# Optimization experiments

Measured on AMD Instinct MI355X. Metric: run time of the kernel, lower is better.

## Reference

```python
import jax, jax.numpy as jnp
import numpy as np

N_NODES = 50000
N_EDGES = 1_600_000
D_IN, D_HID, D_OUT, K = 128, 50, 10, 5


def setup_inputs() -> dict:
    key = jax.random.key(0)
    ks = jax.random.split(key, 6)
    x = jax.random.normal(ks[0], (N_NODES, D_IN), dtype=jnp.float32)
    edge_index = jax.random.randint(ks[1], (2, N_EDGES), 0, N_NODES, dtype=jnp.int64)
    cheb_w = jax.random.normal(ks[2], (K, D_IN, D_HID), dtype=jnp.float32) * 0.05
    cheb_b = jax.random.normal(ks[3], (D_HID,), dtype=jnp.float32) * 0.05
    fc_w = jax.random.normal(ks[4], (D_HID, D_OUT), dtype=jnp.float32) * 0.1
    fc_b = jax.random.normal(ks[5], (D_OUT,), dtype=jnp.float32) * 0.1
    return {"x": x, "edge_index": edge_index, "cheb_w": cheb_w,
            "cheb_b": cheb_b, "fc_w": fc_w, "fc_b": fc_b}


def reference(x, edge_index, cheb_w, cheb_b, fc_w, fc_b):
    # ChebConv (PyG, normalization='sym', lambda_max=2.0):
    # L_hat = 2L/lambda_max - I = -D^{-1/2} A D^{-1/2} (zero diagonal)
    row, col = edge_index[0], edge_index[1]
    n = x.shape[0]
    deg = jax.ops.segment_sum(jnp.ones_like(row, dtype=x.dtype), row, num_segments=n)
    dinv = jnp.where(deg > 0, jax.lax.rsqrt(jnp.maximum(deg, 1.0)), 0.0)
    w = -dinv[row] * dinv[col]  # [E] edge weights of L_hat

    def prop(h):  # L_hat @ h via gather-scale-scatter
        return jax.ops.segment_sum(w[:, None] * h[col], row, num_segments=n)

    tx0 = x
    tx1 = prop(x)
    out = jnp.einsum('ni,io->no', tx0, cheb_w[0]) + jnp.einsum('ni,io->no', tx1, cheb_w[1])
    for k in range(2, K):
        tx2 = 2.0 * prop(tx1) - tx0
        out = out + jnp.einsum('ni,io->no', tx2, cheb_w[k])
        tx0, tx1 = tx1, tx2
    out = out + cheb_b

    h = jax.nn.relu(out)
    logits = h @ fc_w + fc_b
    return jax.nn.log_softmax(logits, axis=1)
```

## Files before the change

kernel.cpp:

```cpp
#include <hip/hip_runtime.h>
#include <hip/hip_fp16.h>

#define N_NODES 50000
#define N_EDGES 1600000
#define D_IN    128
#define D_HID   50
#define D_OUT   10
#define K_CHEB  5

#define P1_BLOCKS 256
#define EPB       (N_EDGES / P1_BLOCKS)
#define NBUCK2    256
#define NB_USED2  196
#define BCAP2     96

#define WH_ELEMS  (K_CHEB * 64 * D_IN)
#define WH_BLOCKS ((WH_ELEMS + 255) / 256)
#define XH_BLOCKS (N_NODES * D_IN / 8 / 256)

#define VROW      64
#define VSTRIDE   ((size_t)(N_NODES + 1) * VROW)

#define NGROUP    (N_NODES / 16)
#define VG_SPAN   512
#define VG_WAVES  (K_CHEB * VG_SPAN)
#define VG_BLOCKS (VG_WAVES / 4)

typedef _Float16 half8_t __attribute__((ext_vector_type(8)));
typedef float    f32x4_t __attribute__((ext_vector_type(4)));


__global__ __launch_bounds__(256) void prep_kernel(const float* __restrict__ x,
                                                   const float* __restrict__ W,
                                                   __half* __restrict__ xh,
                                                   __half* __restrict__ Wh,
                                                   __half* __restrict__ u,
                                                   __half* __restrict__ b1,
                                                   __half* __restrict__ b3,
                                                   __half* __restrict__ b2,
                                                   float* __restrict__ dinv) {
    int tid = threadIdx.x;
    int blk = blockIdx.x;
    if (blk < XH_BLOCKS) {
        size_t base = ((size_t)blk * 256 + tid) * 8;
        float4 a = *(const float4*)(x + base);
        float4 b = *(const float4*)(x + base + 4);
        half8_t h;
        h[0] = (_Float16)a.x; h[1] = (_Float16)a.y;
        h[2] = (_Float16)a.z; h[3] = (_Float16)a.w;
        h[4] = (_Float16)b.x; h[5] = (_Float16)b.y;
        h[6] = (_Float16)b.z; h[7] = (_Float16)b.w;
        *(half8_t*)(xh + base) = h;
    } else if (blk < XH_BLOCKS + WH_BLOCKS) {
        int idx = (blk - XH_BLOCKS) * 256 + tid;
        if (idx < WH_ELEMS) {
            int i = idx & 127;
            int n = (idx >> 7) & 63;
            int t = idx >> 13;
            float vv = (n < D_HID) ? W[t * D_IN * D_HID + i * D_HID + n] : 0.f;
            Wh[idx] = __float2half(vv);
        }
    } else {
        if (tid < VROW) {
            __half z = __float2half(0.f);
            u[4 * VSTRIDE + (size_t)N_NODES * VROW + tid] = z;
            b1[(size_t)N_NODES * VROW + tid] = z;
            b3[(size_t)N_NODES * VROW + tid] = z;
            b2[(size_t)N_NODES * VROW + tid] = z;
        }
        if (tid == 64) dinv[N_NODES] = 0.f;
    }
}

__global__ __launch_bounds__(256) void fused_kernel(const int* __restrict__ row,
                                                    const int* __restrict__ col,
                                                    unsigned int* __restrict__ store,
                                                    int* __restrict__ bcnt,
                                                    const __half* __restrict__ xh,
                                                    const __half* __restrict__ Wh,
                                                    __half* __restrict__ u) {
    __shared__ int cnt[NBUCK2];
    int tid = threadIdx.x;
    int blk = blockIdx.x;
    if (blk < VG_BLOCKS) {
        int lane = tid & 63;
        int wv = __builtin_amdgcn_readfirstlane(tid >> 6);
        int w = blk * 4 + wv;
        int t = w / VG_SPAN;
        int idx = w - t * VG_SPAN;
        int m = lane & 15;
        int quad = lane >> 4;

        const __half* Wt = Wh + t * (64 * D_IN);
        half8_t afr[4][4];
        #pragma unroll
        for (int ks = 0; ks < 4; ++ks) {
            int ko = ks * 32 + quad * 8;
            #pragma unroll
            for (int jt = 0; jt < 4; ++jt)
                afr[ks][jt] = *(const half8_t*)(Wt + (jt * 16 + m) * D_IN + ko);
        }

        __half* ut = u + t * VSTRIDE;

        half8_t pf[4];
        int g = idx;
        {
            const __half* xr = xh + (size_t)(g * 16 + m) * D_IN;
            #pragma unroll
            for (int ks = 0; ks < 4; ++ks)
                pf[ks] = *(const half8_t*)(xr + ks * 32 + quad * 8);
        }

        for (; g < NGROUP; g += VG_SPAN) {
            int node = g * 16 + m;
            half8_t bfr[4];
            #pragma unroll
            for (int ks = 0; ks < 4; ++ks) bfr[ks] = pf[ks];
            int gn = g + VG_SPAN;
            if (gn < NGROUP) {
                const __half* xr = xh + (size_t)(gn * 16 + m) * D_IN;
                #pragma unroll
                for (int ks = 0; ks < 4; ++ks)
                    pf[ks] = *(const half8_t*)(xr + ks * 32 + quad * 8);
            }
            f32x4_t acc[4];
            #pragma unroll
            for (int jt = 0; jt < 4; ++jt) acc[jt] = (f32x4_t)0.f;
            #pragma unroll
            for (int ks = 0; ks < 4; ++ks)
                #pragma unroll
                for (int jt = 0; jt < 4; ++jt)
                    acc[jt] = __builtin_amdgcn_mfma_f32_16x16x32_f16(afr[ks][jt], bfr[ks], acc[jt], 0, 0, 0);
            __half* dst = ut + (size_t)node * VROW + quad * 4;
            #pragma unroll
            for (int jt = 0; jt < 4; ++jt) {
                __half2 h0 = __float22half2_rn(make_float2(acc[jt][0], acc[jt][1]));
                __half2 h1 = __float22half2_rn(make_float2(acc[jt][2], acc[jt][3]));
                uint2 uu;
                uu.x = *(unsigned int*)&h0;
                uu.y = *(unsigned int*)&h1;
                *(uint2*)(dst + jt * 16) = uu;
            }
        }
        return;
    }
    int blk2 = blk - VG_BLOCKS;
    cnt[tid] = 0;
    __syncthreads();
    int base = blk2 * EPB;
    size_t sb = (size_t)blk2 * (NBUCK2 * BCAP2);
    for (int i = tid; i < EPB; i += 256) {
        int r = row[base + i];
        int c = col[base + i];
        int b = r >> 8;
        int pos = atomicAdd(&cnt[b], 1);
        if (pos >= BCAP2) pos = BCAP2 - 1;
        store[sb + b * BCAP2 + pos] = ((unsigned int)(r & 255) << 16) | (unsigned int)c;
    }
    __syncthreads();
    bcnt[blk2 * NBUCK2 + tid] = cnt[tid];
}

__global__ __launch_bounds__(512) void pass2_kernel(const unsigned int* __restrict__ store,
                                                    const int* __restrict__ bcnt,
                                                    int* __restrict__ row_start,
                                                    float* __restrict__ dinv,
                                                    float* __restrict__ dinv2,
                                                    float* __restrict__ sdeg,
                                                    int* __restrict__ ewc) {
    __shared__ int hist[256];
    __shared__ int off[256];
    __shared__ int fill[256];
    __shared__ int sb_part[512];
    __shared__ int pscan[256];
    __shared__ int s_bbase;
    int tid = threadIdx.x;
    int b = blockIdx.x;

    {
        int bt = tid & 255, seg = tid >> 8;
        int sum = 0;
        for (int s = seg * 128; s < seg * 128 + 128; ++s) sum += bcnt[s * NBUCK2 + bt];
        sb_part[tid] = sum;
    }
    __syncthreads();
    if (tid < 256) pscan[tid] = sb_part[tid] + sb_part[256 + tid];
    __syncthreads();
    for (int o = 1; o < 256; o <<= 1) {
        int vv = (tid < 256 && tid >= o) ? pscan[tid - o] : 0;
        __syncthreads();
        if (tid < 256) pscan[tid] += vv;
        __syncthreads();
    }
    if (tid == 0) {
        s_bbase = (b == 0) ? 0 : pscan[b - 1];
        if (b == 0) row_start[N_NODES] = pscan[255];
    }
    if (tid < 256) hist[tid] = 0;
    __syncthreads();
    int bbase_b = s_bbase;

    int strip = tid >> 1;
    int sub   = tid & 1;
    int sn = bcnt[strip * NBUCK2 + b];
    size_t sb = (size_t)strip * (NBUCK2 * BCAP2) + b * BCAP2;
    for (int i = sub; i < sn; i += 2)
        atomicAdd(&hist[store[sb + i] >> 16], 1);
    __syncthreads();
    int d = (tid < 256) ? hist[tid] : 0;
    if (tid < 256) off[tid] = d;
    __syncthreads();
    for (int o = 1; o < 256; o <<= 1) {
        int vv = (tid < 256 && tid >= o) ? off[tid - o] : 0;
        __syncthreads();
        if (tid < 256) off[tid] += vv;
        __syncthreads();
    }
    if (tid < 256) {
        int excl = off[tid] - d + bbase_b;
        hist[tid] = excl;
        fill[tid] = 0;
        int r = (b << 8) + tid;
        if (r < N_NODES) {
            row_start[r] = excl;
            float fd = (float)d;
            dinv[r]  = d ? rsqrtf(fd)  : 0.f;
            dinv2[r] = d ? (1.f / fd)  : 0.f;
            sdeg[r]  = d ? sqrtf(fd)   : 0.f;
        }
    }
    __syncthreads();
    for (int i = sub; i < sn; i += 2) {
        unsigned int vv = store[sb + i];
        int rl = vv >> 16;
        int c = vv & 0xffff;
        int p = atomicAdd(&fill[rl], 1);
        ewc[hist[rl] + p] = c;
    }
}

template<int SCALE_SRC, int DO_SUB, int SCALE_SUB>
__global__ __launch_bounds__(512) void prop_kernel(const int* __restrict__ row_start,
                                                   const int* __restrict__ ewc,
                                                   const float* __restrict__ dinv2,
                                                   const float* __restrict__ dinv,
                                                   const __half* __restrict__ src,
                                                   const __half* __restrict__ addv,
                                                   const __half* __restrict__ subv,
                                                   float alphaM,
                                                   __half* __restrict__ dst) {
    int tid = threadIdx.x;
    int lane = tid & 63;
    int wv = __builtin_amdgcn_readfirstlane(tid >> 6);
    int r = blockIdx.x * 8 + wv;
    int e0 = row_start[r], e1 = row_start[r + 1];
    float fac = -alphaM * dinv2[r];
    int l = lane & 7;
    int g = lane >> 3;
    const uint4* src16 = (const uint4*)src;
    float ac[8];
    #pragma unroll
    for (int j = 0; j < 8; ++j) ac[j] = 0.f;
    for (int e = e0; e < e1; e += 32) {
        #pragma unroll
        for (int i = 0; i < 4; ++i) {
            int base = e + 8 * i;
            int cl = ewc[base + g];
            if (base + g >= e1) cl = N_NODES;
            uint4 uu = src16[(size_t)cl * 8 + l];
            float2 f0 = __half22float2(*(__half2*)&uu.x);
            float2 f1 = __half22float2(*(__half2*)&uu.y);
            float2 f2 = __half22float2(*(__half2*)&uu.z);
            float2 f3 = __half22float2(*(__half2*)&uu.w);
            if (SCALE_SRC) {
                float dc = dinv[cl];
                ac[0] = fmaf(dc, f0.x, ac[0]); ac[1] = fmaf(dc, f0.y, ac[1]);
                ac[2] = fmaf(dc, f1.x, ac[2]); ac[3] = fmaf(dc, f1.y, ac[3]);
                ac[4] = fmaf(dc, f2.x, ac[4]); ac[5] = fmaf(dc, f2.y, ac[5]);
                ac[6] = fmaf(dc, f3.x, ac[6]); ac[7] = fmaf(dc, f3.y, ac[7]);
            } else {
                ac[0] += f0.x; ac[1] += f0.y; ac[2] += f1.x; ac[3] += f1.y;
                ac[4] += f2.x; ac[5] += f2.y; ac[6] += f3.x; ac[7] += f3.y;
            }
        }
    }
    #pragma unroll
    for (int k = 8; k <= 32; k <<= 1) {
        #pragma unroll
        for (int j = 0; j < 8; ++j) ac[j] += __shfl_xor(ac[j], k);
    }
    if (g == 0) {
        float sa = dinv[r];
        size_t o = (size_t)r * 8 + l;
        uint4 av = ((const uint4*)addv)[o];
        float2 av0 = __half22float2(*(__half2*)&av.x);
        float2 av1 = __half22float2(*(__half2*)&av.y);
        float2 av2 = __half22float2(*(__half2*)&av.z);
        float2 av3 = __half22float2(*(__half2*)&av.w);
        float r0 = fmaf(sa, av0.x, fac * ac[0]);
        float r1 = fmaf(sa, av0.y, fac * ac[1]);
        float r2 = fmaf(sa, av1.x, fac * ac[2]);
        float r3 = fmaf(sa, av1.y, fac * ac[3]);
        float r4 = fmaf(sa, av2.x, fac * ac[4]);
        float r5 = fmaf(sa, av2.y, fac * ac[5]);
        float r6 = fmaf(sa, av3.x, fac * ac[6]);
        float r7 = fmaf(sa, av3.y, fac * ac[7]);
        if (DO_SUB) {
            float ss = SCALE_SUB ? dinv[r] : 1.f;
            uint4 sv = ((const uint4*)subv)[o];
            float2 sv0 = __half22float2(*(__half2*)&sv.x);
            float2 sv1 = __half22float2(*(__half2*)&sv.y);
            float2 sv2 = __half22float2(*(__half2*)&sv.z);
            float2 sv3 = __half22float2(*(__half2*)&sv.w);
            r0 = fmaf(-ss, sv0.x, r0); r1 = fmaf(-ss, sv0.y, r1);
            r2 = fmaf(-ss, sv1.x, r2); r3 = fmaf(-ss, sv1.y, r3);
            r4 = fmaf(-ss, sv2.x, r4); r5 = fmaf(-ss, sv2.y, r5);
            r6 = fmaf(-ss, sv3.x, r6); r7 = fmaf(-ss, sv3.y, r7);
        }
        __half2 h0 = __float22half2_rn(make_float2(r0, r1));
        __half2 h1 = __float22half2_rn(make_float2(r2, r3));
        __half2 h2 = __float22half2_rn(make_float2(r4, r5));
        __half2 h3 = __float22half2_rn(make_float2(r6, r7));
        uint4 uu;
        uu.x = *(unsigned int*)&h0;
        uu.y = *(unsigned int*)&h1;
        uu.z = *(unsigned int*)&h2;
        uu.w = *(unsigned int*)&h3;
        ((uint4*)dst)[o] = uu;
    }
}

__global__ __launch_bounds__(256) void final_kernel(const __half* __restrict__ S,
                                                    const float* __restrict__ sdeg,
                                                    const float* __restrict__ cheb_b,
                                                    const float* __restrict__ fc_w,
                                                    const float* __restrict__ fc_b,
                                                    float* __restrict__ out) {
    int r = blockIdx.x * blockDim.x + threadIdx.x;
    if (r >= N_NODES) return;
    float sc = sdeg[r];
    const __half2* s2 = (const __half2*)(S + (size_t)r * VROW);
    float h[D_HID];
    #pragma unroll
    for (int i = 0; i < D_HID / 2; ++i) {
        float2 f = __half22float2(s2[i]);
        float v0 = sc * f.x + cheb_b[2 * i];
        float v1 = sc * f.y + cheb_b[2 * i + 1];
        h[2 * i]     = v0 > 0.f ? v0 : 0.f;
        h[2 * i + 1] = v1 > 0.f ? v1 : 0.f;
    }
    float lg[D_OUT];
    #pragma unroll
    for (int o = 0; o < D_OUT; ++o) lg[o] = fc_b[o];
    #pragma unroll 2
    for (int i = 0; i < D_HID; ++i) {
        float hv = h[i];
        #pragma unroll
        for (int o = 0; o < D_OUT; ++o) lg[o] += hv * fc_w[i * D_OUT + o];
    }
    float mx = lg[0];
    #pragma unroll
    for (int o = 1; o < D_OUT; ++o) mx = fmaxf(mx, lg[o]);
    float s = 0.f;
    #pragma unroll
    for (int o = 0; o < D_OUT; ++o) s += __expf(lg[o] - mx);
    float ls = __logf(s);
    size_t oo = (size_t)r * D_OUT;
    #pragma unroll
    for (int o = 0; o < D_OUT; ++o) out[oo + o] = lg[o] - mx - ls;
}

extern "C" void kernel_launch(void* const* d_in, const int* in_sizes, int n_in,
                              void* d_out, int out_size, void* d_ws, size_t ws_size,
                              hipStream_t stream) {
    const float* x      = (const float*)d_in[0];
    const int*   edge   = (const int*)d_in[1];
    const float* cheb_w = (const float*)d_in[2];
    const float* cheb_b = (const float*)d_in[3];
    const float* fc_w   = (const float*)d_in[4];
    const float* fc_b   = (const float*)d_in[5];
    float* out = (float*)d_out;

    const int* erow = edge;
    const int* ecol = edge + N_EDGES;

    uintptr_t p = ((uintptr_t)d_ws + 255) & ~(uintptr_t)255;
    auto alloc = [&](size_t bytes) {
        uintptr_t q = p;
        p = (p + bytes + 255) & ~(uintptr_t)255;
        return (void*)q;
    };
    unsigned int* store = (unsigned int*)alloc((size_t)P1_BLOCKS * NBUCK2 * BCAP2 * 4);
    int*    bcnt      = (int*)alloc((size_t)P1_BLOCKS * NBUCK2 * 4);
    int*    row_start = (int*)alloc((size_t)(N_NODES + 1) * 4);
    float*  dinv      = (float*)alloc((size_t)(N_NODES + 1) * 4);
    float*  dinv2     = (float*)alloc((size_t)N_NODES * 4);
    float*  sdeg      = (float*)alloc((size_t)N_NODES * 4);
    int*    ewc       = (int*)alloc((size_t)(N_EDGES + 32) * 4);
    __half* Wh        = (__half*)alloc((size_t)WH_ELEMS * 2);
    __half* xh        = (__half*)alloc((size_t)N_NODES * D_IN * 2);
    __half* Sbuf      = (__half*)alloc(VSTRIDE * 2);
    __half* u         = (__half*)alloc(5 * VSTRIDE * 2);
    __half* b1        = (__half*)alloc(VSTRIDE * 2);
    __half* b3        = (__half*)alloc(VSTRIDE * 2);
    __half* b2        = (__half*)alloc(VSTRIDE * 2);
    __half* S  = Sbuf;

    prep_kernel<<<XH_BLOCKS + WH_BLOCKS + 1, 256, 0, stream>>>(
        x, cheb_w, xh, Wh, u, b1, b3, b2, dinv);

    fused_kernel<<<VG_BLOCKS + P1_BLOCKS, 256, 0, stream>>>(
        erow, ecol, store, bcnt, xh, Wh, u);

    pass2_kernel<<<NB_USED2, 512, 0, stream>>>(store, bcnt, row_start,
                                               dinv, dinv2, sdeg, ewc);

    __half* u0 = u;
    __half* u1 = u + 1 * VSTRIDE;
    __half* u2 = u + 2 * VSTRIDE;
    __half* u3 = u + 3 * VSTRIDE;
    __half* u4 = u + 4 * VSTRIDE;
    const int PB = N_NODES / 8;
    prop_kernel<1, 0, 0><<<PB, 512, 0, stream>>>(row_start, ewc, dinv2, dinv,
                                                 u4, u3, u3, 2.f, b3);
    prop_kernel<0, 1, 1><<<PB, 512, 0, stream>>>(row_start, ewc, dinv2, dinv,
                                                 b3, u2, u4, 2.f, b2);
    prop_kernel<0, 1, 0><<<PB, 512, 0, stream>>>(row_start, ewc, dinv2, dinv,
                                                 b2, u1, b3, 2.f, b1);
    prop_kernel<0, 1, 0><<<PB, 512, 0, stream>>>(row_start, ewc, dinv2, dinv,
                                                 b1, u0, b2, 1.f, S);

    final_kernel<<<(N_NODES + 255) / 256, 256, 0, stream>>>(S, sdeg, cheb_b,
                                                            fc_w, fc_b, out);
}
```

Before: 282.5 us.

## Build CSR via global degree histogram, single-block scan, and atomic scatter

Replaces the two-pass bucketed CSR construction (per-block local buckets, then per-bucket histogram, scan and fill) with a global-atomic degree histogram fused into the prep kernel. A single-block scan kernel then computes row_start and cursors, and the fused kernel scatters columns using per-row global atomics, alongside the degree normalisation. This removes the large bucket store and the pass2 kernel, but adds a memset, a one-block scan launch, and many contended global atomics. Edge order within each row becomes nondeterministic, which can change floating-point summation order.

```diff
diff --git a/kernel.cpp b/kernel.cpp
--- a/kernel.cpp
+++ b/kernel.cpp
@@ -8,15 +8,19 @@
 #define D_OUT   10
 #define K_CHEB  5
 
-#define P1_BLOCKS 256
-#define EPB       (N_EDGES / P1_BLOCKS)
-#define NBUCK2    256
-#define NB_USED2  196
-#define BCAP2     96
-
 #define WH_ELEMS  (K_CHEB * 64 * D_IN)
 #define WH_BLOCKS ((WH_ELEMS + 255) / 256)
 #define XH_BLOCKS (N_NODES * D_IN / 8 / 256)
+
+#define HIST_BLOCKS 1250
+#define HIST_EPB    1280
+
+#define DEG_PAD   50048
+#define SCAN_T    782
+
+#define SC_EPB    1024
+#define SC_BLOCKS ((N_EDGES + SC_EPB - 1) / SC_EPB)
+#define DN_BLOCKS ((N_NODES + 255) / 256)
 
 #define VROW      64
 #define VSTRIDE   ((size_t)(N_NODES + 1) * VROW)
@@ -32,13 +36,15 @@
 
 __global__ __launch_bounds__(256) void prep_kernel(const float* __restrict__ x,
                                                    const float* __restrict__ W,
+                                                   const int* __restrict__ row,
                                                    __half* __restrict__ xh,
                                                    __half* __restrict__ Wh,
                                                    __half* __restrict__ u,
                                                    __half* __restrict__ b1,
                                                    __half* __restrict__ b3,
                                                    __half* __restrict__ b2,
-                                                   float* __restrict__ dinv) {
+                                                   float* __restrict__ dinv,
+                                                   int* __restrict__ deg) {
     int tid = threadIdx.x;
     int blk = blockIdx.x;
     if (blk < XH_BLOCKS) {
@@ -60,7 +66,7 @@
             float vv = (n < D_HID) ? W[t * D_IN * D_HID + i * D_HID + n] : 0.f;
             Wh[idx] = __float2half(vv);
         }
-    } else {
+    } else if (blk == XH_BLOCKS + WH_BLOCKS) {
         if (tid < VROW) {
             __half z = __float2half(0.f);
             u[4 * VSTRIDE + (size_t)N_NODES * VROW + tid] = z;
@@ -69,17 +75,67 @@
             b2[(size_t)N_NODES * VROW + tid] = z;
         }
         if (tid == 64) dinv[N_NODES] = 0.f;
-    }
+    } else {
+        int hb = blk - (XH_BLOCKS + WH_BLOCKS + 1);
+        int base = hb * HIST_EPB;
+        for (int i = tid; i < HIST_EPB; i += 256)
+            atomicAdd(&deg[row[base + i]], 1);
+    }
+}
+
+__global__ __launch_bounds__(1024) void scan_kernel(const int* __restrict__ deg,
+                                                    int* __restrict__ row_start,
+                                                    int* __restrict__ cursor) {
+    __shared__ int part[1024];
+    int tid = threadIdx.x;
+    int sum = 0;
+    if (tid < SCAN_T) {
+        const uint4* d4 = (const uint4*)deg + (size_t)tid * 16;
+        #pragma unroll
+        for (int i = 0; i < 16; ++i) {
+            uint4 v = d4[i];
+            sum += (int)v.x + (int)v.y + (int)v.z + (int)v.w;
+        }
+    }
+    part[tid] = sum;
+    __syncthreads();
+    for (int o = 1; o < 1024; o <<= 1) {
+        int v = (tid >= o) ? part[tid - o] : 0;
+        __syncthreads();
+        part[tid] += v;
+        __syncthreads();
+    }
+    if (tid < SCAN_T) {
+        int run = (tid == 0) ? 0 : part[tid - 1];
+        const uint4* d4 = (const uint4*)deg + (size_t)tid * 16;
+        uint4* rs4 = (uint4*)row_start + (size_t)tid * 16;
+        uint4* cu4 = (uint4*)cursor + (size_t)tid * 16;
+        int ng = (tid == SCAN_T - 1) ? 4 : 16;
+        for (int i = 0; i < ng; ++i) {
+            uint4 v = d4[i];
+            uint4 o4;
+            o4.x = (unsigned)run; run += (int)v.x;
+            o4.y = (unsigned)run; run += (int)v.y;
+            o4.z = (unsigned)run; run += (int)v.z;
+            o4.w = (unsigned)run; run += (int)v.w;
+            rs4[i] = o4;
+            cu4[i] = o4;
+        }
+    }
+    if (tid == 0) row_start[N_NODES] = part[1023];
 }
 
 __global__ __launch_bounds__(256) void fused_kernel(const int* __restrict__ row,
                                                     const int* __restrict__ col,
-                                                    unsigned int* __restrict__ store,
-                                                    int* __restrict__ bcnt,
+                                                    int* __restrict__ cursor,
+                                                    int* __restrict__ ewc,
                                                     const __half* __restrict__ xh,
                                                     const __half* __restrict__ Wh,
-                                                    __half* __restrict__ u) {
-    __shared__ int cnt[NBUCK2];
+                                                    __half* __restrict__ u,
+                                                    const int* __restrict__ deg,
+                                                    float* __restrict__ dinv,
+                                                    float* __restrict__ dinv2,
+                                                    float* __restrict__ sdeg) {
     int tid = threadIdx.x;
     int blk = blockIdx.x;
     if (blk < VG_BLOCKS) {
@@ -145,98 +201,28 @@
         }
         return;
     }
-    int blk2 = blk - VG_BLOCKS;
-    cnt[tid] = 0;
-    __syncthreads();
-    int base = blk2 * EPB;
-    size_t sb = (size_t)blk2 * (NBUCK2 * BCAP2);
-    for (int i = tid; i < EPB; i += 256) {
-        int r = row[base + i];
-        int c = col[base + i];
-        int b = r >> 8;
-        int pos = atomicAdd(&cnt[b], 1);
-        if (pos >= BCAP2) pos = BCAP2 - 1;
-        store[sb + b * BCAP2 + pos] = ((unsigned int)(r & 255) << 16) | (unsigned int)c;
-    }
-    __syncthreads();
-    bcnt[blk2 * NBUCK2 + tid] = cnt[tid];
-}
-
-__global__ __launch_bounds__(512) void pass2_kernel(const unsigned int* __restrict__ store,
-                                                    const int* __restrict__ bcnt,
-                                                    int* __restrict__ row_start,
-                                                    float* __restrict__ dinv,
-                                                    float* __restrict__ dinv2,
-                                                    float* __restrict__ sdeg,
-                                                    int* __restrict__ ewc) {
-    __shared__ int hist[256];
-    __shared__ int off[256];
-    __shared__ int fill[256];
-    __shared__ int sb_part[512];
-    __shared__ int pscan[256];
-    __shared__ int s_bbase;
-    int tid = threadIdx.x;
-    int b = blockIdx.x;
-
-    {
-        int bt = tid & 255, seg = tid >> 8;
-        int sum = 0;
-        for (int s = seg * 128; s < seg * 128 + 128; ++s) sum += bcnt[s * NBUCK2 + bt];
-        sb_part[tid] = sum;
-    }
-    __syncthreads();
-    if (tid < 256) pscan[tid] = sb_part[tid] + sb_part[256 + tid];
-    __syncthreads();
-    for (int o = 1; o < 256; o <<= 1) {
-        int vv = (tid < 256 && tid >= o) ? pscan[tid - o] : 0;
-        __syncthreads();
-        if (tid < 256) pscan[tid] += vv;
-        __syncthreads();
-    }
-    if (tid == 0) {
-        s_bbase = (b == 0) ? 0 : pscan[b - 1];
-        if (b == 0) row_start[N_NODES] = pscan[255];
-    }
-    if (tid < 256) hist[tid] = 0;
-    __syncthreads();
-    int bbase_b = s_bbase;
-
-    int strip = tid >> 1;
-    int sub   = tid & 1;
-    int sn = bcnt[strip * NBUCK2 + b];
-    size_t sb = (size_t)strip * (NBUCK2 * BCAP2) + b * BCAP2;
-    for (int i = sub; i < sn; i += 2)
-        atomicAdd(&hist[store[sb + i] >> 16], 1);
-    __syncthreads();
-    int d = (tid < 256) ? hist[tid] : 0;
-    if (tid < 256) off[tid] = d;
-    __syncthreads();
-    for (int o = 1; o < 256; o <<= 1) {
-        int vv = (tid < 256 && tid >= o) ? off[tid - o] : 0;
-        __syncthreads();
-        if (tid < 256) off[tid] += vv;
-        __syncthreads();
-    }
-    if (tid < 256) {
-        int excl = off[tid] - d + bbase_b;
-        hist[tid] = excl;
-        fill[tid] = 0;
-        int r = (b << 8) + tid;
-        if (r < N_NODES) {
-            row_start[r] = excl;
-            float fd = (float)d;
-            dinv[r]  = d ? rsqrtf(fd)  : 0.f;
-            dinv2[r] = d ? (1.f / fd)  : 0.f;
-            sdeg[r]  = d ? sqrtf(fd)   : 0.f;
-        }
-    }
-    __syncthreads();
-    for (int i = sub; i < sn; i += 2) {
-        unsigned int vv = store[sb + i];
-        int rl = vv >> 16;
-        int c = vv & 0xffff;
-        int p = atomicAdd(&fill[rl], 1);
-        ewc[hist[rl] + p] = c;
+    if (blk < VG_BLOCKS + SC_BLOCKS) {
+        int sb = blk - VG_BLOCKS;
+        int base = sb * SC_EPB;
+        #pragma unroll
+        for (int i = 0; i < SC_EPB / 256; ++i) {
+            int e = base + i * 256 + tid;
+            if (e < N_EDGES) {
+                int r = row[e];
+                int c = col[e];
+                int pos = atomicAdd(&cursor[r], 1);
+                ewc[pos] = c;
+            }
+        }
+        return;
+    }
+    int node = (blk - VG_BLOCKS - SC_BLOCKS) * 256 + tid;
+    if (node < N_NODES) {
+        int d = deg[node];
+        float fd = (float)d;
+        dinv[node]  = d ? rsqrtf(fd) : 0.f;
+        dinv2[node] = d ? (1.f / fd) : 0.f;
+        sdeg[node]  = d ? sqrtf(fd)  : 0.f;
     }
 }
 
@@ -391,8 +377,8 @@
         p = (p + bytes + 255) & ~(uintptr_t)255;
         return (void*)q;
     };
-    unsigned int* store = (unsigned int*)alloc((size_t)P1_BLOCKS * NBUCK2 * BCAP2 * 4);
-    int*    bcnt      = (int*)alloc((size_t)P1_BLOCKS * NBUCK2 * 4);
+    int*    deg       = (int*)alloc((size_t)DEG_PAD * 4);
+    int*    cursor    = (int*)alloc((size_t)N_NODES * 4);
     int*    row_start = (int*)alloc((size_t)(N_NODES + 1) * 4);
     float*  dinv      = (float*)alloc((size_t)(N_NODES + 1) * 4);
     float*  dinv2     = (float*)alloc((size_t)N_NODES * 4);
@@ -407,14 +393,15 @@
     __half* b2        = (__half*)alloc(VSTRIDE * 2);
     __half* S  = Sbuf;
 
-    prep_kernel<<<XH_BLOCKS + WH_BLOCKS + 1, 256, 0, stream>>>(
-        x, cheb_w, xh, Wh, u, b1, b3, b2, dinv);
-
-    fused_kernel<<<VG_BLOCKS + P1_BLOCKS, 256, 0, stream>>>(
-        erow, ecol, store, bcnt, xh, Wh, u);
-
-    pass2_kernel<<<NB_USED2, 512, 0, stream>>>(store, bcnt, row_start,
-                                               dinv, dinv2, sdeg, ewc);
+    hipMemsetAsync(deg, 0, (size_t)DEG_PAD * 4, stream);
+
+    prep_kernel<<<XH_BLOCKS + WH_BLOCKS + 1 + HIST_BLOCKS, 256, 0, stream>>>(
+        x, cheb_w, erow, xh, Wh, u, b1, b3, b2, dinv, deg);
+
+    scan_kernel<<<1, 1024, 0, stream>>>(deg, row_start, cursor);
+
+    fused_kernel<<<VG_BLOCKS + SC_BLOCKS + DN_BLOCKS, 256, 0, stream>>>(
+        erow, ecol, cursor, ewc, xh, Wh, u, deg, dinv, dinv2, sdeg);
 
     __half* u0 = u;
     __half* u1 = u + 1 * VSTRIDE;
```

New measurement: 453.2 us. 60.4% more time.

## Regroup edge bucketing with prep and CSR build with MFMA projection

Applied to the files above, without the earlier changes.

Edge bucketing now runs in the same launch as the x/W fp16 conversion, and the CSR-building pass now shares a launch with the MFMA projection of x by the Chebyshev weights. This removes one kernel launch and lets independent work overlap within each launch. Bucketing uses 512 blocks with half the per-bucket capacity, so each pass-2 thread scans one strip serially. The prop kernel's edge unroll is also halved. The smaller bucket capacity raises the risk of overflow clamping if a block's bucket exceeds 48 entries.

```diff
diff --git a/kernel.cpp b/kernel.cpp
--- a/kernel.cpp
+++ b/kernel.cpp
@@ -8,41 +8,64 @@
 #define D_OUT   10
 #define K_CHEB  5
 
-#define P1_BLOCKS 256
-#define EPB       (N_EDGES / P1_BLOCKS)
-#define NBUCK2    256
-#define NB_USED2  196
-#define BCAP2     96
-
 #define WH_ELEMS  (K_CHEB * 64 * D_IN)
 #define WH_BLOCKS ((WH_ELEMS + 255) / 256)
 #define XH_BLOCKS (N_NODES * D_IN / 8 / 256)
 
+#define P1S_BLOCKS 512
+#define EPB        (N_EDGES / P1S_BLOCKS)
+#define NBUCK      256
+#define NB_USED    196
+#define BCAP       48
+
 #define VROW      64
 #define VSTRIDE   ((size_t)(N_NODES + 1) * VROW)
 
 #define NGROUP    (N_NODES / 16)
 #define VG_SPAN   512
 #define VG_WAVES  (K_CHEB * VG_SPAN)
-#define VG_BLOCKS (VG_WAVES / 4)
+#define VGB_BLOCKS (VG_WAVES / 8)
 
 typedef _Float16 half8_t __attribute__((ext_vector_type(8)));
 typedef float    f32x4_t __attribute__((ext_vector_type(4)));
 
 
-__global__ __launch_bounds__(256) void prep_kernel(const float* __restrict__ x,
-                                                   const float* __restrict__ W,
-                                                   __half* __restrict__ xh,
-                                                   __half* __restrict__ Wh,
-                                                   __half* __restrict__ u,
-                                                   __half* __restrict__ b1,
-                                                   __half* __restrict__ b3,
-                                                   __half* __restrict__ b2,
-                                                   float* __restrict__ dinv) {
+__global__ __launch_bounds__(256) void buildA_kernel(const int* __restrict__ row,
+                                                     const int* __restrict__ col,
+                                                     unsigned int* __restrict__ store,
+                                                     int* __restrict__ bcnt,
+                                                     const float* __restrict__ x,
+                                                     const float* __restrict__ W,
+                                                     __half* __restrict__ xh,
+                                                     __half* __restrict__ Wh,
+                                                     __half* __restrict__ u,
+                                                     __half* __restrict__ b1,
+                                                     __half* __restrict__ b3,
+                                                     __half* __restrict__ b2,
+                                                     float* __restrict__ dinv) {
+    __shared__ int cnt[NBUCK];
     int tid = threadIdx.x;
     int blk = blockIdx.x;
-    if (blk < XH_BLOCKS) {
-        size_t base = ((size_t)blk * 256 + tid) * 8;
+    if (blk < P1S_BLOCKS) {
+        cnt[tid] = 0;
+        __syncthreads();
+        int base = blk * EPB;
+        size_t sb = (size_t)blk * (NBUCK * BCAP);
+        for (int i = tid; i < EPB; i += 256) {
+            int r = row[base + i];
+            int c = col[base + i];
+            int b = r >> 8;
+            int pos = atomicAdd(&cnt[b], 1);
+            if (pos >= BCAP) pos = BCAP - 1;
+            store[sb + b * BCAP + pos] = ((unsigned int)(r & 255) << 16) | (unsigned int)c;
+        }
+        __syncthreads();
+        bcnt[blk * NBUCK + tid] = cnt[tid];
+        return;
+    }
+    int pb = blk - P1S_BLOCKS;
+    if (pb < XH_BLOCKS) {
+        size_t base = ((size_t)pb * 256 + tid) * 8;
         float4 a = *(const float4*)(x + base);
         float4 b = *(const float4*)(x + base + 4);
         half8_t h;
@@ -51,8 +74,8 @@
         h[4] = (_Float16)b.x; h[5] = (_Float16)b.y;
         h[6] = (_Float16)b.z; h[7] = (_Float16)b.w;
         *(half8_t*)(xh + base) = h;
-    } else if (blk < XH_BLOCKS + WH_BLOCKS) {
-        int idx = (blk - XH_BLOCKS) * 256 + tid;
+    } else if (pb < XH_BLOCKS + WH_BLOCKS) {
+        int idx = (pb - XH_BLOCKS) * 256 + tid;
         if (idx < WH_ELEMS) {
             int i = idx & 127;
             int n = (idx >> 7) & 63;
@@ -72,20 +95,28 @@
     }
 }
 
-__global__ __launch_bounds__(256) void fused_kernel(const int* __restrict__ row,
-                                                    const int* __restrict__ col,
-                                                    unsigned int* __restrict__ store,
-                                                    int* __restrict__ bcnt,
-                                                    const __half* __restrict__ xh,
-                                                    const __half* __restrict__ Wh,
-                                                    __half* __restrict__ u) {
-    __shared__ int cnt[NBUCK2];
+__global__ __launch_bounds__(512) void buildB_kernel(const unsigned int* __restrict__ store,
+                                                     const int* __restrict__ bcnt,
+                                                     int* __restrict__ row_start,
+                                                     float* __restrict__ dinv,
+                                                     float* __restrict__ dinv2,
+                                                     float* __restrict__ sdeg,
+                                                     int* __restrict__ ewc,
+                                                     const __half* __restrict__ xh,
+                                                     const __half* __restrict__ Wh,
+                                                     __half* __restrict__ u) {
+    __shared__ int hist[256];
+    __shared__ int off[256];
+    __shared__ int fill[256];
+    __shared__ int sb_part[512];
+    __shared__ int pscan[256];
+    __shared__ int s_bbase;
     int tid = threadIdx.x;
     int blk = blockIdx.x;
-    if (blk < VG_BLOCKS) {
+    if (blk >= NB_USED) {
         int lane = tid & 63;
         int wv = __builtin_amdgcn_readfirstlane(tid >> 6);
-        int w = blk * 4 + wv;
+        int w = (blk - NB_USED) * 8 + wv;
         int t = w / VG_SPAN;
         int idx = w - t * VG_SPAN;
         int m = lane & 15;
@@ -145,43 +176,11 @@
         }
         return;
     }
-    int blk2 = blk - VG_BLOCKS;
-    cnt[tid] = 0;
-    __syncthreads();
-    int base = blk2 * EPB;
-    size_t sb = (size_t)blk2 * (NBUCK2 * BCAP2);
-    for (int i = tid; i < EPB; i += 256) {
-        int r = row[base + i];
-        int c = col[base + i];
-        int b = r >> 8;
-        int pos = atomicAdd(&cnt[b], 1);
-        if (pos >= BCAP2) pos = BCAP2 - 1;
-        store[sb + b * BCAP2 + pos] = ((unsigned int)(r & 255) << 16) | (unsigned int)c;
-    }
-    __syncthreads();
-    bcnt[blk2 * NBUCK2 + tid] = cnt[tid];
-}
-
-__global__ __launch_bounds__(512) void pass2_kernel(const unsigned int* __restrict__ store,
-                                                    const int* __restrict__ bcnt,
-                                                    int* __restrict__ row_start,
-                                                    float* __restrict__ dinv,
-                                                    float* __restrict__ dinv2,
-                                                    float* __restrict__ sdeg,
-                                                    int* __restrict__ ewc) {
-    __shared__ int hist[256];
-    __shared__ int off[256];
-    __shared__ int fill[256];
-    __shared__ int sb_part[512];
-    __shared__ int pscan[256];
-    __shared__ int s_bbase;
-    int tid = threadIdx.x;
-    int b = blockIdx.x;
-
+    int b = blk;
     {
         int bt = tid & 255, seg = tid >> 8;
         int sum = 0;
-        for (int s = seg * 128; s < seg * 128 + 128; ++s) sum += bcnt[s * NBUCK2 + bt];
+        for (int s = seg * 256; s < seg * 256 + 256; ++s) sum += bcnt[s * NBUCK + bt];
         sb_part[tid] = sum;
     }
     __syncthreads();
@@ -201,11 +200,10 @@
     __syncthreads();
     int bbase_b = s_bbase;
 
-    int strip = tid >> 1;
-    int sub   = tid & 1;
-    int sn = bcnt[strip * NBUCK2 + b];
-    size_t sb = (size_t)strip * (NBUCK2 * BCAP2) + b * BCAP2;
-    for (int i = sub; i < sn; i += 2)
+    int strip = tid;
+    int sn = bcnt[strip * NBUCK + b];
+    size_t sb = (size_t)strip * (NBUCK * BCAP) + b * BCAP;
+    for (int i = 0; i < sn; ++i)
         atomicAdd(&hist[store[sb + i] >> 16], 1);
     __syncthreads();
     int d = (tid < 256) ? hist[tid] : 0;
@@ -231,7 +229,7 @@
         }
     }
     __syncthreads();
-    for (int i = sub; i < sn; i += 2) {
+    for (int i = 0; i < sn; ++i) {
         unsigned int vv = store[sb + i];
         int rl = vv >> 16;
         int c = vv & 0xffff;
@@ -262,9 +260,9 @@
     float ac[8];
     #pragma unroll
     for (int j = 0; j < 8; ++j) ac[j] = 0.f;
-    for (int e = e0; e < e1; e += 32) {
+    for (int e = e0; e < e1; e += 16) {
         #pragma unroll
-        for (int i = 0; i < 4; ++i) {
+        for (int i = 0; i < 2; ++i) {
             int base = e + 8 * i;
             int cl = ewc[base + g];
             if (base + g >= e1) cl = N_NODES;
@@ -391,13 +389,13 @@
         p = (p + bytes + 255) & ~(uintptr_t)255;
         return (void*)q;
     };
-    unsigned int* store = (unsigned int*)alloc((size_t)P1_BLOCKS * NBUCK2 * BCAP2 * 4);
-    int*    bcnt      = (int*)alloc((size_t)P1_BLOCKS * NBUCK2 * 4);
     int*    row_start = (int*)alloc((size_t)(N_NODES + 1) * 4);
     float*  dinv      = (float*)alloc((size_t)(N_NODES + 1) * 4);
     float*  dinv2     = (float*)alloc((size_t)N_NODES * 4);
     float*  sdeg      = (float*)alloc((size_t)N_NODES * 4);
     int*    ewc       = (int*)alloc((size_t)(N_EDGES + 32) * 4);
+    unsigned int* store = (unsigned int*)alloc((size_t)P1S_BLOCKS * NBUCK * BCAP * 4);
+    int*    bcnt      = (int*)alloc((size_t)P1S_BLOCKS * NBUCK * 4);
     __half* Wh        = (__half*)alloc((size_t)WH_ELEMS * 2);
     __half* xh        = (__half*)alloc((size_t)N_NODES * D_IN * 2);
     __half* Sbuf      = (__half*)alloc(VSTRIDE * 2);
@@ -407,14 +405,11 @@
     __half* b2        = (__half*)alloc(VSTRIDE * 2);
     __half* S  = Sbuf;
 
-    prep_kernel<<<XH_BLOCKS + WH_BLOCKS + 1, 256, 0, stream>>>(
-        x, cheb_w, xh, Wh, u, b1, b3, b2, dinv);
-
-    fused_kernel<<<VG_BLOCKS + P1_BLOCKS, 256, 0, stream>>>(
-        erow, ecol, store, bcnt, xh, Wh, u);
-
-    pass2_kernel<<<NB_USED2, 512, 0, stream>>>(store, bcnt, row_start,
-                                               dinv, dinv2, sdeg, ewc);
+    buildA_kernel<<<P1S_BLOCKS + XH_BLOCKS + WH_BLOCKS + 1, 256, 0, stream>>>(
+        erow, ecol, store, bcnt, x, cheb_w, xh, Wh, u, b1, b3, b2, dinv);
+
+    buildB_kernel<<<NB_USED + VGB_BLOCKS, 512, 0, stream>>>(
+        store, bcnt, row_start, dinv, dinv2, sdeg, ewc, xh, Wh, u);
 
     __half* u0 = u;
     __half* u1 = u + 1 * VSTRIDE;
```

Result: slower. 295.0 us (+4.4%).
